# Kernel optimization log

Hardware: AMD Instinct MI355X
Metric: run time of the kernel (lower is better)

The kernel has to match this reference:

```python
import jax, jax.numpy as jnp
import numpy as np

N = 30000      # num nodes
E = 600000     # num edges
D = 128        # feature dim (all layers)
R = 7          # num_relation
G = 16         # num graphs in batch
L = 3          # num layers (hidden_dims = [128,128,128])


def setup_inputs() -> dict:
    key = jax.random.key(0)
    ks = jax.random.split(key, 10)
    x = jax.random.normal(ks[0], (N, D), dtype=jnp.float32)
    node_in = jax.random.randint(ks[1], (E,), 0, N)
    node_out = jax.random.randint(ks[2], (E,), 0, N)
    relation = jax.random.randint(ks[3], (E,), 0, R)
    edge_weight = jax.random.uniform(ks[4], (E,), dtype=jnp.float32)
    node2graph = jnp.sort(jax.random.randint(ks[5], (N,), 0, G))
    # learned params: per-layer relational linear (R*D -> D) and self-loop linear (D -> D)
    Wr = jax.random.normal(ks[6], (L, R * D, D), dtype=jnp.float32) * 0.02
    br = jnp.zeros((L, D), dtype=jnp.float32)
    Wl = jax.random.normal(ks[7], (L, D, D), dtype=jnp.float32) * 0.02
    bl = jnp.zeros((L, D), dtype=jnp.float32)
    return dict(x=x, node_in=node_in, node_out=node_out, relation=relation,
                edge_weight=edge_weight, node2graph=node2graph,
                Wr=Wr, br=br, Wl=Wl, bl=bl)


def reference(x, node_in, node_out, relation, edge_weight, node2graph, Wr, br, Wl, bl):
    # relation-indexed destination segment: node_out * R + relation
    seg = node_out * R + relation            # (E,)
    ew = edge_weight[:, None]                # (E, 1)
    h = x
    for i in range(L):
        msg = h[node_in] * ew                                         # gather + weight, (E, D)
        upd = jax.ops.segment_sum(msg, seg, num_segments=N * R)       # scatter_add, (N*R, D)
        upd = upd.reshape(N, R * D)                                   # per-relation concat
        h = jax.nn.relu(upd @ Wr[i] + br[i] + h @ Wl[i] + bl[i])      # linear + self-loop + act
    node_feature = h                                                  # (N, D)
    graph_feature = jax.ops.segment_sum(node_feature, node2graph, num_segments=G)  # sum readout
    return graph_feature, node_feature
```

## Files before the change

kernel.cpp:

```cpp
#include <hip/hip_runtime.h>
#include <hip/hip_bf16.h>

#define NN 30000
#define NE 600000
#define DD 128
#define RR 7
#define GG 16
#define LL 3

#define NB64 ((NN + 63) / 64)

typedef short bf16x8 __attribute__((ext_vector_type(8)));
typedef float f32x4  __attribute__((ext_vector_type(4)));

__device__ __forceinline__ unsigned short f2bf(float f) {
    unsigned u = __float_as_uint(f);
    unsigned r = (u + 0x7fffu + ((u >> 16) & 1u)) >> 16;
    return (unsigned short)r;
}
__device__ __forceinline__ float bf2f(unsigned short b) {
    return __uint_as_float(((unsigned)b) << 16);
}
__device__ __forceinline__ ushort2 pk2bf(float a, float b) {
    __hip_bfloat162 t = __float22bfloat162_rn(make_float2(a, b));
    return *(ushort2*)&t;
}

__device__ __forceinline__ void gl_lds16(const void* g, void* l) {
    __builtin_amdgcn_global_load_lds(
        (const __attribute__((address_space(1))) void*)g,
        (__attribute__((address_space(3))) void*)l, 16, 0, 0);
}

__global__ __launch_bounds__(256) void pack_weights(
    const float* __restrict__ Wl,
    const float* __restrict__ Wr,
    unsigned short* __restrict__ Bw2)
{
    int t = blockIdx.x * 256 + threadIdx.x;
    if (t >= LL * 131072) return;
    int l    = t >> 17;
    int rem  = t & 131071;
    int ch   = rem >> 14;
    int c    = (rem >> 7) & 127;
    int kkin = rem & 127;
    float v;
    if (ch == 0) {
        v = Wl[(size_t)l * 16384 + kkin * 128 + c];
    } else {
        v = Wr[(size_t)l * 114688 + (size_t)((ch - 1) * 128 + kkin) * 128 + c];
    }
    Bw2[t] = f2bf(v);
}

__global__ __launch_bounds__(256) void convert_bf16(
    const float* __restrict__ in, unsigned short* __restrict__ out, int n4)
{
    int i = blockIdx.x * 256 + threadIdx.x;
    if (i >= n4) return;
    float4 v = ((const float4*)in)[i];
    ushort2 lo = pk2bf(v.x, v.y);
    ushort2 hi = pk2bf(v.z, v.w);
    ((ushort4*)out)[i] = make_ushort4(lo.x, lo.y, hi.x, hi.y);
}

__global__ __launch_bounds__(256) void bucket_hist(
    const int* __restrict__ node_out, int* __restrict__ bcnt, int E)
{
    int e = blockIdx.x * 256 + threadIdx.x;
    if (e < E) atomicAdd(&bcnt[(node_out[e] >> 6) * 16], 1);
}

__global__ __launch_bounds__(512) void bucket_scan(
    const int* __restrict__ bcnt, int* __restrict__ bstart,
    int* __restrict__ bcur, int nb)
{
    __shared__ int s[512];
    int t = threadIdx.x;
    int v = (t < nb) ? bcnt[t * 16] : 0;
    s[t] = v;
    __syncthreads();
#pragma unroll
    for (int off = 1; off < 512; off <<= 1) {
        int u = (t >= off) ? s[t - off] : 0;
        __syncthreads();
        s[t] += u;
        __syncthreads();
    }
    if (t <= nb) {
        int excl = s[t] - v;
        bstart[t] = excl;
        if (t < nb) bcur[t * 16] = excl;
    }
}

__global__ __launch_bounds__(256) void bucket_scatter(
    const int* __restrict__ node_in,
    const int* __restrict__ node_out,
    const int* __restrict__ relation,
    const float* __restrict__ ew,
    int* __restrict__ bcur,
    int2* __restrict__ tmp,
    int E)
{
    int e = blockIdx.x * 256 + threadIdx.x;
    if (e >= E) return;
    int o = node_out[e];
    int pos = atomicAdd(&bcur[(o >> 6) * 16], 1);
    tmp[pos] = make_int2(((o & 63) << 18) | (node_in[e] << 3) | relation[e],
                         __float_as_int(ew[e]));
}

__global__ __launch_bounds__(256) void bucket_sort(
    const int2* __restrict__ tmp,
    const int* __restrict__ bstart,
    int2* __restrict__ meta,
    int* __restrict__ start,
    int N)
{
    __shared__ int hist[64];
    __shared__ int scan[64];
    __shared__ int cur[64];
    const int b = blockIdx.x;
    const int t = threadIdx.x;
    const int s0 = bstart[b];
    const int s1 = bstart[b + 1];

    if (t < 64) hist[t] = 0;
    __syncthreads();
    for (int i = s0 + t; i < s1; i += 256)
        atomicAdd(&hist[((unsigned)tmp[i].x) >> 18], 1);
    __syncthreads();

    int v = (t < 64) ? hist[t] : 0;
    if (t < 64) scan[t] = v;
    __syncthreads();
#pragma unroll
    for (int off = 1; off < 64; off <<= 1) {
        int u = (t < 64 && t >= off) ? scan[t - off] : 0;
        __syncthreads();
        if (t < 64) scan[t] += u;
        __syncthreads();
    }
    if (t < 64) {
        int excl = scan[t] - v;
        cur[t] = s0 + excl;
        int node = b * 64 + t;
        if (node <= N) start[node] = s0 + excl;
    }
    __syncthreads();

    for (int i = s0 + t; i < s1; i += 256) {
        int2 m = tmp[i];
        int j = ((unsigned)m.x) >> 18;
        int pos = atomicAdd(&cur[j], 1);
        meta[pos] = make_int2(m.x & 0x3ffff, m.y);
    }
}

__global__ __launch_bounds__(256) void aggregate_h(
    const unsigned short* __restrict__ hb,
    const int* __restrict__ start,
    const int2* __restrict__ meta,
    unsigned short* __restrict__ upd,
    int N)
{
    int wid = (blockIdx.x * 256 + threadIdx.x) >> 6;
    int lane = threadIdx.x & 63;
    if (wid >= N) return;

    int e0 = start[wid];
    int e1 = start[wid + 1];

    float ax[7], ay[7];
#pragma unroll
    for (int r = 0; r < 7; ++r) { ax[r] = 0.f; ay[r] = 0.f; }

#define GATHER(m) (*(const unsigned*)(hb + (((size_t)((m).x >> 3)) << 7) + lane * 2))
#define ACCUM(m, u) do {                                                       \
    float w_  = __int_as_float((m).y);                                         \
    float hx_ = __uint_as_float((u) << 16);                                    \
    float hy_ = __uint_as_float((u) & 0xffff0000u);                            \
    switch (__builtin_amdgcn_readfirstlane((m).x) & 7) {                       \
      case 0: ax[0]=fmaf(w_,hx_,ax[0]); ay[0]=fmaf(w_,hy_,ay[0]); break;       \
      case 1: ax[1]=fmaf(w_,hx_,ax[1]); ay[1]=fmaf(w_,hy_,ay[1]); break;       \
      case 2: ax[2]=fmaf(w_,hx_,ax[2]); ay[2]=fmaf(w_,hy_,ay[2]); break;       \
      case 3: ax[3]=fmaf(w_,hx_,ax[3]); ay[3]=fmaf(w_,hy_,ay[3]); break;       \
      case 4: ax[4]=fmaf(w_,hx_,ax[4]); ay[4]=fmaf(w_,hy_,ay[4]); break;       \
      case 5: ax[5]=fmaf(w_,hx_,ax[5]); ay[5]=fmaf(w_,hy_,ay[5]); break;       \
      default: ax[6]=fmaf(w_,hx_,ax[6]); ay[6]=fmaf(w_,hy_,ay[6]); break;      \
    } } while (0)

    int e = e0;
    for (; e + 4 <= e1; e += 4) {
        int2 m0 = meta[e + 0], m1 = meta[e + 1];
        int2 m2 = meta[e + 2], m3 = meta[e + 3];
        unsigned u0 = GATHER(m0), u1 = GATHER(m1);
        unsigned u2 = GATHER(m2), u3 = GATHER(m3);
        ACCUM(m0, u0); ACCUM(m1, u1); ACCUM(m2, u2); ACCUM(m3, u3);
    }
    for (; e < e1; ++e) {
        int2 m = meta[e];
        unsigned u = GATHER(m);
        ACCUM(m, u);
    }
#undef GATHER
#undef ACCUM

    unsigned short* urow = upd + (size_t)wid * 896 + lane * 2;
#pragma unroll
    for (int r = 0; r < 7; ++r) {
        ushort2 p = pk2bf(ax[r], ay[r]);
        *(unsigned*)(urow + r * 128) = ((unsigned)p.y << 16) | p.x;
    }
}

__global__ __launch_bounds__(256) void gemm_fused(
    const unsigned short* __restrict__ hb,
    const unsigned short* __restrict__ upd,
    const unsigned short* __restrict__ Bw2,
    const float* __restrict__ br,
    const float* __restrict__ bl,
    unsigned short* __restrict__ hout,
    float* __restrict__ nf,
    int N)
{
    __shared__ unsigned short As[64 * 128];
    __shared__ unsigned short Bs[128 * 128];

    const int tid  = threadIdx.x;
    const int wave = tid >> 6;
    const int lane = tid & 63;
    const int quad = lane >> 4;
    const int l16  = lane & 15;
    const int row0 = blockIdx.x * 64;

    const int lr = lane >> 4;
    const int ls = lane & 15;

    f32x4 acc[4][2];
#pragma unroll
    for (int mt = 0; mt < 4; ++mt)
#pragma unroll
        for (int nt = 0; nt < 2; ++nt)
            acc[mt][nt] = (f32x4){0.f, 0.f, 0.f, 0.f};

    const unsigned short* As_l = As + l16 * 128;
    const unsigned short* Bs_l = Bs + (wave * 32 + l16) * 128;
    const int swz = l16 & 7;

    for (int ch = 0; ch < 8; ++ch) {
#pragma unroll
        for (int i = 0; i < 4; ++i) {
            int g = i * 4 + wave;
            int r = g * 4 + lr;
            int slot = ls ^ (r & 7);
            const unsigned short* src;
            if (ch == 0)
                src = hb + (size_t)(row0 + r) * 128 + slot * 8;
            else
                src = upd + (size_t)(row0 + r) * 896 + (ch - 1) * 128 + slot * 8;
            gl_lds16(src, As + g * 512);
        }
        const unsigned short* Bchunk = Bw2 + (size_t)ch * 16384;
#pragma unroll
        for (int i = 0; i < 8; ++i) {
            int g = i * 4 + wave;
            int r = g * 4 + lr;
            int slot = ls ^ (r & 7);
            gl_lds16(Bchunk + (size_t)r * 128 + slot * 8, Bs + g * 512);
        }
        __syncthreads();

#pragma unroll
        for (int kc = 0; kc < 4; ++kc) {
            int so = ((kc * 4 + quad) ^ swz) * 8;
            bf16x8 a0 = *(const bf16x8*)(As_l + 0 * 16 * 128 + so);
            bf16x8 a1 = *(const bf16x8*)(As_l + 1 * 16 * 128 + so);
            bf16x8 a2 = *(const bf16x8*)(As_l + 2 * 16 * 128 + so);
            bf16x8 a3 = *(const bf16x8*)(As_l + 3 * 16 * 128 + so);
            bf16x8 b0 = *(const bf16x8*)(Bs_l + 0 * 16 * 128 + so);
            bf16x8 b1 = *(const bf16x8*)(Bs_l + 1 * 16 * 128 + so);
            acc[0][0] = __builtin_amdgcn_mfma_f32_16x16x32_bf16(a0, b0, acc[0][0], 0, 0, 0);
            acc[1][0] = __builtin_amdgcn_mfma_f32_16x16x32_bf16(a1, b0, acc[1][0], 0, 0, 0);
            acc[2][0] = __builtin_amdgcn_mfma_f32_16x16x32_bf16(a2, b0, acc[2][0], 0, 0, 0);
            acc[3][0] = __builtin_amdgcn_mfma_f32_16x16x32_bf16(a3, b0, acc[3][0], 0, 0, 0);
            acc[0][1] = __builtin_amdgcn_mfma_f32_16x16x32_bf16(a0, b1, acc[0][1], 0, 0, 0);
            acc[1][1] = __builtin_amdgcn_mfma_f32_16x16x32_bf16(a1, b1, acc[1][1], 0, 0, 0);
            acc[2][1] = __builtin_amdgcn_mfma_f32_16x16x32_bf16(a2, b1, acc[2][1], 0, 0, 0);
            acc[3][1] = __builtin_amdgcn_mfma_f32_16x16x32_bf16(a3, b1, acc[3][1], 0, 0, 0);
        }
        __syncthreads();
    }

    const int ncol = wave * 32 + l16;
    float bias0 = br[ncol] + bl[ncol];
    float bias1 = br[ncol + 16] + bl[ncol + 16];
#pragma unroll
    for (int mt = 0; mt < 4; ++mt) {
#pragma unroll
        for (int reg = 0; reg < 4; ++reg) {
            int row = row0 + mt * 16 + quad * 4 + reg;
            if (row < N) {
                float v0 = fmaxf(acc[mt][0][reg] + bias0, 0.f);
                float v1 = fmaxf(acc[mt][1][reg] + bias1, 0.f);
                if (hout) {
                    ushort2 p = pk2bf(v0, v1);
                    hout[(size_t)row * DD + ncol]      = p.x;
                    hout[(size_t)row * DD + ncol + 16] = p.y;
                }
                if (nf) {
                    nf[(size_t)row * DD + ncol]      = v0;
                    nf[(size_t)row * DD + ncol + 16] = v1;
                }
            }
        }
    }
}

__global__ __launch_bounds__(256) void graph_sum(
    const float* __restrict__ nf,
    const int* __restrict__ n2g,
    float* __restrict__ gf,
    int N)
{
    int t = blockIdx.x * 256 + threadIdx.x;
    int chunk = t >> 5;
    int lane = t & 31;
    int n0 = chunk * 16;
    if (n0 >= N) return;
    int nend = n0 + 16; if (nend > N) nend = N;

    float4 acc = make_float4(0.f, 0.f, 0.f, 0.f);
    int curg = n2g[n0];
    for (int n = n0; n < nend; ++n) {
        int g = n2g[n];
        if (g != curg) {
            float* dst = gf + (size_t)curg * DD + lane * 4;
            atomicAdd(dst + 0, acc.x); atomicAdd(dst + 1, acc.y);
            atomicAdd(dst + 2, acc.z); atomicAdd(dst + 3, acc.w);
            acc = make_float4(0.f, 0.f, 0.f, 0.f);
            curg = g;
        }
        float4 v = *(const float4*)(nf + (size_t)n * DD + lane * 4);
        acc.x += v.x; acc.y += v.y; acc.z += v.z; acc.w += v.w;
    }
    float* dst = gf + (size_t)curg * DD + lane * 4;
    atomicAdd(dst + 0, acc.x); atomicAdd(dst + 1, acc.y);
    atomicAdd(dst + 2, acc.z); atomicAdd(dst + 3, acc.w);
}

extern "C" void kernel_launch(void* const* d_in, const int* in_sizes, int n_in,
                              void* d_out, int out_size, void* d_ws, size_t ws_size,
                              hipStream_t stream)
{
    const float* x        = (const float*)d_in[0];
    const int*   node_in  = (const int*)d_in[1];
    const int*   node_out = (const int*)d_in[2];
    const int*   relation = (const int*)d_in[3];
    const float* ew       = (const float*)d_in[4];
    const int*   n2g      = (const int*)d_in[5];
    const float* Wr       = (const float*)d_in[6];
    const float* br       = (const float*)d_in[7];
    const float* Wl       = (const float*)d_in[8];
    const float* bl       = (const float*)d_in[9];

    float* out = (float*)d_out;
    float* gf = out;
    float* nf = out + GG * DD;

    char* w = (char*)d_ws;
    unsigned short* upd  = (unsigned short*)w; w += (size_t)NN * RR * DD * 2;
    unsigned short* hbA  = (unsigned short*)w; w += (size_t)NN * DD * 2;
    unsigned short* hbB  = (unsigned short*)w; w += (size_t)NN * DD * 2;
    unsigned short* Bw2  = (unsigned short*)w; w += (size_t)LL * 131072 * 2;
    int2*  meta   = (int2*)w;                  w += (size_t)NE * 8;
    int2*  tmp    = (int2*)w;                  w += (size_t)NE * 8;
    int*   start  = (int*)w;                   w += (size_t)(NN + 1) * 4 + 60;
    int*   bcnt   = (int*)w;                   w += (size_t)NB64 * 16 * 4 + 64;
    int*   bcur   = (int*)w;                   w += (size_t)NB64 * 16 * 4 + 64;
    int*   bstart = (int*)w;                   w += (size_t)(NB64 + 1) * 4 + 60;

    const int N = NN, E = NE;

    pack_weights<<<(LL * 131072 + 255) / 256, 256, 0, stream>>>(Wl, Wr, Bw2);
    convert_bf16<<<(N * DD / 4 + 255) / 256, 256, 0, stream>>>(x, hbA, N * DD / 4);

    hipMemsetAsync(bcnt, 0, (size_t)NB64 * 16 * sizeof(int), stream);
    bucket_hist<<<(E + 255) / 256, 256, 0, stream>>>(node_out, bcnt, E);
    bucket_scan<<<1, 512, 0, stream>>>(bcnt, bstart, bcur, NB64);
    bucket_scatter<<<(E + 255) / 256, 256, 0, stream>>>(
        node_in, node_out, relation, ew, bcur, tmp, E);
    bucket_sort<<<NB64, 256, 0, stream>>>(tmp, bstart, meta, start, N);

    unsigned short* hin = hbA;
    unsigned short* hnext = hbB;
    for (int l = 0; l < LL; ++l) {
        const float* br_l = br + (size_t)l * DD;
        const float* bl_l = bl + (size_t)l * DD;
        const unsigned short* Bw2_l = Bw2 + (size_t)l * 131072;
        bool last = (l == LL - 1);

        aggregate_h<<<(N * 64 + 255) / 256, 256, 0, stream>>>(
            hin, start, meta, upd, N);

        gemm_fused<<<(N + 63) / 64, 256, 0, stream>>>(
            hin, upd, Bw2_l, br_l, bl_l,
            last ? (unsigned short*)nullptr : hnext,
            last ? nf : (float*)nullptr, N);

        unsigned short* t = hin; hin = hnext; hnext = t;
    }

    hipMemsetAsync(gf, 0, (size_t)GG * DD * sizeof(float), stream);
    int chunks = (N + 15) / 16;
    graph_sum<<<(chunks * 32 + 255) / 256, 256, 0, stream>>>(nf, n2g, gf, N);
}
```

Before: 358.1 us.

## Fuse relational aggregation into the GEMM kernel, sorting edges by relation per block

Replaces the separate aggregate and GEMM kernels with one per-64-node-block kernel. For each relation, the kernel gathers neighbour features into an fp32 LDS tile using shared-memory atomics, converts the tile to bf16, and runs that relation's MFMA chunk. Edges are now bucket-sorted by (relation, local node) within each block, so every wave walks a contiguous per-relation range. This removes the N×7×128 upd buffer's global write and read, at the cost of LDS atomics, more barriers, and gather latency sitting inside the GEMM block with less overlap.

```diff
diff --git a/kernel.cpp b/kernel.cpp
--- a/kernel.cpp
+++ b/kernel.cpp
@@ -18,9 +18,6 @@
     unsigned r = (u + 0x7fffu + ((u >> 16) & 1u)) >> 16;
     return (unsigned short)r;
 }
-__device__ __forceinline__ float bf2f(unsigned short b) {
-    return __uint_as_float(((unsigned)b) << 16);
-}
 __device__ __forceinline__ ushort2 pk2bf(float a, float b) {
     __hip_bfloat162 t = __float22bfloat162_rn(make_float2(a, b));
     return *(ushort2*)&t;
@@ -35,22 +32,22 @@
 __global__ __launch_bounds__(256) void pack_weights(
     const float* __restrict__ Wl,
     const float* __restrict__ Wr,
-    unsigned short* __restrict__ Bw2)
+    unsigned short* __restrict__ Bw)
 {
     int t = blockIdx.x * 256 + threadIdx.x;
-    if (t >= LL * 131072) return;
-    int l    = t >> 17;
-    int rem  = t & 131071;
-    int ch   = rem >> 14;
-    int c    = (rem >> 7) & 127;
-    int kkin = rem & 127;
+    if (t >= LL * 1024 * DD) return;
+    int l = t >> 17;
+    int rem = t & 131071;
+    int n = rem >> 7;
+    int k = rem & 127;
     float v;
-    if (ch == 0) {
-        v = Wl[(size_t)l * 16384 + kkin * 128 + c];
+    if (n < DD) {
+        v = Wl[(size_t)l * DD * DD + k * DD + n];
     } else {
-        v = Wr[(size_t)l * 114688 + (size_t)((ch - 1) * 128 + kkin) * 128 + c];
-    }
-    Bw2[t] = f2bf(v);
+        int q = n - DD;
+        v = Wr[(size_t)l * RR * DD * DD + (size_t)((q >> 7) * DD + k) * DD + (q & 127)];
+    }
+    Bw[(size_t)l * 1024 * DD + n * DD + k] = f2bf(v);
 }
 
 __global__ __launch_bounds__(256) void convert_bf16(
@@ -111,121 +108,69 @@
                          __float_as_int(ew[e]));
 }
 
-__global__ __launch_bounds__(256) void bucket_sort(
+__global__ __launch_bounds__(512) void bucket_sort(
     const int2* __restrict__ tmp,
     const int* __restrict__ bstart,
     int2* __restrict__ meta,
-    int* __restrict__ start,
-    int N)
-{
-    __shared__ int hist[64];
-    __shared__ int scan[64];
-    __shared__ int cur[64];
+    int* __restrict__ rstart,
+    int NB)
+{
+    __shared__ int hist[512];
+    __shared__ int scan[512];
+    __shared__ int cur[512];
     const int b = blockIdx.x;
     const int t = threadIdx.x;
     const int s0 = bstart[b];
     const int s1 = bstart[b + 1];
 
-    if (t < 64) hist[t] = 0;
-    __syncthreads();
-    for (int i = s0 + t; i < s1; i += 256)
-        atomicAdd(&hist[((unsigned)tmp[i].x) >> 18], 1);
-    __syncthreads();
-
-    int v = (t < 64) ? hist[t] : 0;
-    if (t < 64) scan[t] = v;
-    __syncthreads();
-#pragma unroll
-    for (int off = 1; off < 64; off <<= 1) {
-        int u = (t < 64 && t >= off) ? scan[t - off] : 0;
-        __syncthreads();
-        if (t < 64) scan[t] += u;
-        __syncthreads();
-    }
-    if (t < 64) {
-        int excl = scan[t] - v;
-        cur[t] = s0 + excl;
-        int node = b * 64 + t;
-        if (node <= N) start[node] = s0 + excl;
-    }
-    __syncthreads();
-
-    for (int i = s0 + t; i < s1; i += 256) {
+    hist[t] = 0;
+    __syncthreads();
+    for (int i = s0 + t; i < s1; i += 512) {
+        int k = tmp[i].x;
+        int bin = ((k & 7) << 6) | ((unsigned)k >> 18);
+        atomicAdd(&hist[bin], 1);
+    }
+    __syncthreads();
+
+    int v = hist[t];
+    scan[t] = v;
+    __syncthreads();
+#pragma unroll
+    for (int off = 1; off < 512; off <<= 1) {
+        int u = (t >= off) ? scan[t - off] : 0;
+        __syncthreads();
+        scan[t] += u;
+        __syncthreads();
+    }
+    int excl = scan[t] - v;
+    cur[t] = s0 + excl;
+    if ((t & 63) == 0) rstart[b * 8 + (t >> 6)] = s0 + excl;
+    if (t == 511 && b == NB - 1) rstart[NB * 8] = s1;
+    __syncthreads();
+
+    for (int i = s0 + t; i < s1; i += 512) {
         int2 m = tmp[i];
-        int j = ((unsigned)m.x) >> 18;
-        int pos = atomicAdd(&cur[j], 1);
-        meta[pos] = make_int2(m.x & 0x3ffff, m.y);
-    }
-}
-
-__global__ __launch_bounds__(256) void aggregate_h(
+        int k = m.x;
+        int bin = ((k & 7) << 6) | ((unsigned)k >> 18);
+        int pos = atomicAdd(&cur[bin], 1);
+        int in = (k >> 3) & 0x7fff;
+        meta[pos] = make_int2((in << 6) | ((unsigned)k >> 18), m.y);
+    }
+}
+
+__global__ __launch_bounds__(512) void layer_fused(
     const unsigned short* __restrict__ hb,
-    const int* __restrict__ start,
+    const unsigned short* __restrict__ Bw,
+    const int* __restrict__ rstart,
     const int2* __restrict__ meta,
-    unsigned short* __restrict__ upd,
-    int N)
-{
-    int wid = (blockIdx.x * 256 + threadIdx.x) >> 6;
-    int lane = threadIdx.x & 63;
-    if (wid >= N) return;
-
-    int e0 = start[wid];
-    int e1 = start[wid + 1];
-
-    float ax[7], ay[7];
-#pragma unroll
-    for (int r = 0; r < 7; ++r) { ax[r] = 0.f; ay[r] = 0.f; }
-
-#define GATHER(m) (*(const unsigned*)(hb + (((size_t)((m).x >> 3)) << 7) + lane * 2))
-#define ACCUM(m, u) do {                                                       \
-    float w_  = __int_as_float((m).y);                                         \
-    float hx_ = __uint_as_float((u) << 16);                                    \
-    float hy_ = __uint_as_float((u) & 0xffff0000u);                            \
-    switch (__builtin_amdgcn_readfirstlane((m).x) & 7) {                       \
-      case 0: ax[0]=fmaf(w_,hx_,ax[0]); ay[0]=fmaf(w_,hy_,ay[0]); break;       \
-      case 1: ax[1]=fmaf(w_,hx_,ax[1]); ay[1]=fmaf(w_,hy_,ay[1]); break;       \
-      case 2: ax[2]=fmaf(w_,hx_,ax[2]); ay[2]=fmaf(w_,hy_,ay[2]); break;       \
-      case 3: ax[3]=fmaf(w_,hx_,ax[3]); ay[3]=fmaf(w_,hy_,ay[3]); break;       \
-      case 4: ax[4]=fmaf(w_,hx_,ax[4]); ay[4]=fmaf(w_,hy_,ay[4]); break;       \
-      case 5: ax[5]=fmaf(w_,hx_,ax[5]); ay[5]=fmaf(w_,hy_,ay[5]); break;       \
-      default: ax[6]=fmaf(w_,hx_,ax[6]); ay[6]=fmaf(w_,hy_,ay[6]); break;      \
-    } } while (0)
-
-    int e = e0;
-    for (; e + 4 <= e1; e += 4) {
-        int2 m0 = meta[e + 0], m1 = meta[e + 1];
-        int2 m2 = meta[e + 2], m3 = meta[e + 3];
-        unsigned u0 = GATHER(m0), u1 = GATHER(m1);
-        unsigned u2 = GATHER(m2), u3 = GATHER(m3);
-        ACCUM(m0, u0); ACCUM(m1, u1); ACCUM(m2, u2); ACCUM(m3, u3);
-    }
-    for (; e < e1; ++e) {
-        int2 m = meta[e];
-        unsigned u = GATHER(m);
-        ACCUM(m, u);
-    }
-#undef GATHER
-#undef ACCUM
-
-    unsigned short* urow = upd + (size_t)wid * 896 + lane * 2;
-#pragma unroll
-    for (int r = 0; r < 7; ++r) {
-        ushort2 p = pk2bf(ax[r], ay[r]);
-        *(unsigned*)(urow + r * 128) = ((unsigned)p.y << 16) | p.x;
-    }
-}
-
-__global__ __launch_bounds__(256) void gemm_fused(
-    const unsigned short* __restrict__ hb,
-    const unsigned short* __restrict__ upd,
-    const unsigned short* __restrict__ Bw2,
     const float* __restrict__ br,
     const float* __restrict__ bl,
     unsigned short* __restrict__ hout,
     float* __restrict__ nf,
     int N)
 {
-    __shared__ unsigned short As[64 * 128];
+    __shared__ float          updf[64 * 128];
+    __shared__ unsigned short updb[64 * 128];
     __shared__ unsigned short Bs[128 * 128];
 
     const int tid  = threadIdx.x;
@@ -233,86 +178,142 @@
     const int lane = tid & 63;
     const int quad = lane >> 4;
     const int l16  = lane & 15;
-    const int row0 = blockIdx.x * 64;
-
+    const int b    = blockIdx.x;
+    const int row0 = b * 64;
     const int lr = lane >> 4;
     const int ls = lane & 15;
 
-    f32x4 acc[4][2];
-#pragma unroll
-    for (int mt = 0; mt < 4; ++mt)
-#pragma unroll
-        for (int nt = 0; nt < 2; ++nt)
-            acc[mt][nt] = (f32x4){0.f, 0.f, 0.f, 0.f};
-
-    const unsigned short* As_l = As + l16 * 128;
-    const unsigned short* Bs_l = Bs + (wave * 32 + l16) * 128;
+    {
+        float4 z = {0.f, 0.f, 0.f, 0.f};
+        for (int i = tid; i < 64 * 128 / 4; i += 512) ((float4*)updf)[i] = z;
+    }
+#pragma unroll
+    for (int i = 0; i < 2; ++i) {
+        int g = i * 8 + wave;
+        int r = g * 4 + lr;
+        int slot = ls ^ (r & 7);
+        gl_lds16(hb + (size_t)(row0 + r) * 128 + slot * 8, updb + g * 512);
+    }
+#pragma unroll
+    for (int i = 0; i < 4; ++i) {
+        int g = i * 8 + wave;
+        int r = g * 4 + lr;
+        int slot = ls ^ (r & 7);
+        gl_lds16(Bw + (size_t)r * 128 + slot * 8, Bs + g * 512);
+    }
+    __syncthreads();
+
+    f32x4 acc[4];
+#pragma unroll
+    for (int mt = 0; mt < 4; ++mt) acc[mt] = (f32x4){0.f, 0.f, 0.f, 0.f};
+
+    const unsigned short* As_l = updb + l16 * 128;
+    const unsigned short* Bs_l = Bs + (wave * 16 + l16) * 128;
     const int swz = l16 & 7;
 
-    for (int ch = 0; ch < 8; ++ch) {
+#define GEMM_CHUNK() do {                                                     \
+    _Pragma("unroll")                                                         \
+    for (int kc = 0; kc < 4; ++kc) {                                          \
+        int so = ((kc * 4 + quad) ^ swz) * 8;                                 \
+        bf16x8 bf = *(const bf16x8*)(Bs_l + so);                              \
+        _Pragma("unroll")                                                     \
+        for (int mt = 0; mt < 4; ++mt) {                                      \
+            bf16x8 af = *(const bf16x8*)(As_l + mt * 16 * 128 + so);          \
+            acc[mt] = __builtin_amdgcn_mfma_f32_16x16x32_bf16(af, bf, acc[mt], 0, 0, 0); \
+        }                                                                     \
+    } } while (0)
+
+    GEMM_CHUNK();
+
+    for (int r = 0; r < 7; ++r) {
+        __syncthreads();
+
+        const unsigned short* Bsrc = Bw + (size_t)(r + 1) * 128 * 128;
 #pragma unroll
         for (int i = 0; i < 4; ++i) {
-            int g = i * 4 + wave;
-            int r = g * 4 + lr;
-            int slot = ls ^ (r & 7);
-            const unsigned short* src;
-            if (ch == 0)
-                src = hb + (size_t)(row0 + r) * 128 + slot * 8;
-            else
-                src = upd + (size_t)(row0 + r) * 896 + (ch - 1) * 128 + slot * 8;
-            gl_lds16(src, As + g * 512);
-        }
-        const unsigned short* Bchunk = Bw2 + (size_t)ch * 16384;
-#pragma unroll
-        for (int i = 0; i < 8; ++i) {
-            int g = i * 4 + wave;
-            int r = g * 4 + lr;
-            int slot = ls ^ (r & 7);
-            gl_lds16(Bchunk + (size_t)r * 128 + slot * 8, Bs + g * 512);
-        }
-        __syncthreads();
-
-#pragma unroll
-        for (int kc = 0; kc < 4; ++kc) {
-            int so = ((kc * 4 + quad) ^ swz) * 8;
-            bf16x8 a0 = *(const bf16x8*)(As_l + 0 * 16 * 128 + so);
-            bf16x8 a1 = *(const bf16x8*)(As_l + 1 * 16 * 128 + so);
-            bf16x8 a2 = *(const bf16x8*)(As_l + 2 * 16 * 128 + so);
-            bf16x8 a3 = *(const bf16x8*)(As_l + 3 * 16 * 128 + so);
-            bf16x8 b0 = *(const bf16x8*)(Bs_l + 0 * 16 * 128 + so);
-            bf16x8 b1 = *(const bf16x8*)(Bs_l + 1 * 16 * 128 + so);
-            acc[0][0] = __builtin_amdgcn_mfma_f32_16x16x32_bf16(a0, b0, acc[0][0], 0, 0, 0);
-            acc[1][0] = __builtin_amdgcn_mfma_f32_16x16x32_bf16(a1, b0, acc[1][0], 0, 0, 0);
-            acc[2][0] = __builtin_amdgcn_mfma_f32_16x16x32_bf16(a2, b0, acc[2][0], 0, 0, 0);
-            acc[3][0] = __builtin_amdgcn_mfma_f32_16x16x32_bf16(a3, b0, acc[3][0], 0, 0, 0);
-            acc[0][1] = __builtin_amdgcn_mfma_f32_16x16x32_bf16(a0, b1, acc[0][1], 0, 0, 0);
-            acc[1][1] = __builtin_amdgcn_mfma_f32_16x16x32_bf16(a1, b1, acc[1][1], 0, 0, 0);
-            acc[2][1] = __builtin_amdgcn_mfma_f32_16x16x32_bf16(a2, b1, acc[2][1], 0, 0, 0);
-            acc[3][1] = __builtin_amdgcn_mfma_f32_16x16x32_bf16(a3, b1, acc[3][1], 0, 0, 0);
-        }
-        __syncthreads();
-    }
-
-    const int ncol = wave * 32 + l16;
-    float bias0 = br[ncol] + bl[ncol];
-    float bias1 = br[ncol + 16] + bl[ncol + 16];
+            int g = i * 8 + wave;
+            int rr = g * 4 + lr;
+            int slot = ls ^ (rr & 7);
+            gl_lds16(Bsrc + (size_t)rr * 128 + slot * 8, Bs + g * 512);
+        }
+
+        int rs0 = rstart[b * 8 + r];
+        int rs1 = rstart[b * 8 + r + 1];
+        int len = rs1 - rs0;
+        int e   = rs0 + ((len * wave) >> 3);
+        int ee  = rs0 + ((len * (wave + 1)) >> 3);
+
+        float ax = 0.f, ay = 0.f;
+        int curn = -1;
+        int2 m = make_int2(0, 0);
+        unsigned u = 0;
+        if (e < ee) {
+            m = meta[e];
+            u = *(const unsigned*)(hb + ((size_t)(m.x >> 6) << 7) + lane * 2);
+        }
+        while (e < ee) {
+            int2 m2 = m; unsigned u2 = u;
+            if (e + 1 < ee) {
+                m2 = meta[e + 1];
+                u2 = *(const unsigned*)(hb + ((size_t)(m2.x >> 6) << 7) + lane * 2);
+            }
+            int ln = m.x & 63;
+            if (ln != curn) {
+                if (curn >= 0) {
+                    atomicAdd(&updf[(curn << 7) + lane * 2], ax);
+                    atomicAdd(&updf[(curn << 7) + lane * 2 + 1], ay);
+                }
+                curn = ln; ax = 0.f; ay = 0.f;
+            }
+            float w_ = __int_as_float(m.y);
+            ax = fmaf(w_, __uint_as_float(u << 16), ax);
+            ay = fmaf(w_, __uint_as_float(u & 0xffff0000u), ay);
+            m = m2; u = u2; ++e;
+        }
+        if (curn >= 0) {
+            atomicAdd(&updf[(curn << 7) + lane * 2], ax);
+            atomicAdd(&updf[(curn << 7) + lane * 2 + 1], ay);
+        }
+        __syncthreads();
+
+#pragma unroll
+        for (int i = 0; i < 2; ++i) {
+            int idx = i * 512 + tid;
+            int row = idx >> 4, slot = idx & 15;
+            int wslot = slot ^ (row & 7);
+            float4 f0 = ((const float4*)updf)[row * 32 + slot * 2];
+            float4 f1 = ((const float4*)updf)[row * 32 + slot * 2 + 1];
+            ushort2 p0 = pk2bf(f0.x, f0.y);
+            ushort2 p1 = pk2bf(f0.z, f0.w);
+            ushort2 p2 = pk2bf(f1.x, f1.y);
+            ushort2 p3 = pk2bf(f1.z, f1.w);
+            uint4 o;
+            o.x = (unsigned)p0.x | ((unsigned)p0.y << 16);
+            o.y = (unsigned)p1.x | ((unsigned)p1.y << 16);
+            o.z = (unsigned)p2.x | ((unsigned)p2.y << 16);
+            o.w = (unsigned)p3.x | ((unsigned)p3.y << 16);
+            ((uint4*)updb)[row * 16 + wslot] = o;
+            float4 z = {0.f, 0.f, 0.f, 0.f};
+            ((float4*)updf)[row * 32 + slot * 2]     = z;
+            ((float4*)updf)[row * 32 + slot * 2 + 1] = z;
+        }
+        __syncthreads();
+
+        GEMM_CHUNK();
+    }
+#undef GEMM_CHUNK
+
+    const int col = wave * 16 + l16;
+    float bias = br[col] + bl[col];
 #pragma unroll
     for (int mt = 0; mt < 4; ++mt) {
 #pragma unroll
         for (int reg = 0; reg < 4; ++reg) {
             int row = row0 + mt * 16 + quad * 4 + reg;
             if (row < N) {
-                float v0 = fmaxf(acc[mt][0][reg] + bias0, 0.f);
-                float v1 = fmaxf(acc[mt][1][reg] + bias1, 0.f);
-                if (hout) {
-                    ushort2 p = pk2bf(v0, v1);
-                    hout[(size_t)row * DD + ncol]      = p.x;
-                    hout[(size_t)row * DD + ncol + 16] = p.y;
-                }
-                if (nf) {
-                    nf[(size_t)row * DD + ncol]      = v0;
-                    nf[(size_t)row * DD + ncol + 16] = v1;
-                }
+                float v = fmaxf(acc[mt][reg] + bias, 0.f);
+                if (hout) hout[(size_t)row * DD + col] = f2bf(v);
+                if (nf)   nf[(size_t)row * DD + col] = v;
             }
         }
     }
@@ -370,20 +371,19 @@
     float* nf = out + GG * DD;
 
     char* w = (char*)d_ws;
-    unsigned short* upd  = (unsigned short*)w; w += (size_t)NN * RR * DD * 2;
     unsigned short* hbA  = (unsigned short*)w; w += (size_t)NN * DD * 2;
     unsigned short* hbB  = (unsigned short*)w; w += (size_t)NN * DD * 2;
-    unsigned short* Bw2  = (unsigned short*)w; w += (size_t)LL * 131072 * 2;
+    unsigned short* Bw   = (unsigned short*)w; w += (size_t)LL * 1024 * DD * 2;
     int2*  meta   = (int2*)w;                  w += (size_t)NE * 8;
     int2*  tmp    = (int2*)w;                  w += (size_t)NE * 8;
-    int*   start  = (int*)w;                   w += (size_t)(NN + 1) * 4 + 60;
+    int*   rstart = (int*)w;                   w += (size_t)(NB64 * 8 + 1) * 4 + 60;
     int*   bcnt   = (int*)w;                   w += (size_t)NB64 * 16 * 4 + 64;
     int*   bcur   = (int*)w;                   w += (size_t)NB64 * 16 * 4 + 64;
     int*   bstart = (int*)w;                   w += (size_t)(NB64 + 1) * 4 + 60;
 
     const int N = NN, E = NE;
 
-    pack_weights<<<(LL * 131072 + 255) / 256, 256, 0, stream>>>(Wl, Wr, Bw2);
+    pack_weights<<<(LL * 1024 * DD + 255) / 256, 256, 0, stream>>>(Wl, Wr, Bw);
     convert_bf16<<<(N * DD / 4 + 255) / 256, 256, 0, stream>>>(x, hbA, N * DD / 4);
 
     hipMemsetAsync(bcnt, 0, (size_t)NB64 * 16 * sizeof(int), stream);
@@ -391,21 +391,18 @@
     bucket_scan<<<1, 512, 0, stream>>>(bcnt, bstart, bcur, NB64);
     bucket_scatter<<<(E + 255) / 256, 256, 0, stream>>>(
         node_in, node_out, relation, ew, bcur, tmp, E);
-    bucket_sort<<<NB64, 256, 0, stream>>>(tmp, bstart, meta, start, N);
+    bucket_sort<<<NB64, 512, 0, stream>>>(tmp, bstart, meta, rstart, NB64);
 
     unsigned short* hin = hbA;
     unsigned short* hnext = hbB;
     for (int l = 0; l < LL; ++l) {
         const float* br_l = br + (size_t)l * DD;
         const float* bl_l = bl + (size_t)l * DD;
-        const unsigned short* Bw2_l = Bw2 + (size_t)l * 131072;
+        const unsigned short* Bw_l = Bw + (size_t)l * 1024 * DD;
         bool last = (l == LL - 1);
 
-        aggregate_h<<<(N * 64 + 255) / 256, 256, 0, stream>>>(
-            hin, start, meta, upd, N);
-
-        gemm_fused<<<(N + 63) / 64, 256, 0, stream>>>(
-            hin, upd, Bw2_l, br_l, bl_l,
+        layer_fused<<<NB64, 512, 0, stream>>>(
+            hin, Bw_l, rstart, meta, br_l, bl_l,
             last ? (unsigned short*)nullptr : hnext,
             last ? nf : (float*)nullptr, N);
 
```

Result: slower. 731.1 us (+104.2%).
